# Kernel tuning notes

Measured on AMD Instinct MI355X. Metric: run time of the kernel, lower is better.

## Reference

```python
import jax, jax.numpy as jnp
import numpy as np

N_DIM = 2  # number of trailing feature columns treated as coordinates


def setup_inputs() -> dict:
    key = jax.random.key(0)
    k1, k2, k3, k4 = jax.random.split(key, 4)
    B, N, F, O = 32, 1024, 64, 128
    x = jax.random.normal(k1, (B, N, F), dtype=jnp.float32)
    mask = (jax.random.uniform(k2, (B, N)) < 0.8).astype(jnp.float32)
    # A has shape ((F+1)*2 - 1, O) = (2F+1, O) per build()
    A = jax.random.normal(k3, ((F + 1) * 2 - 1, O), dtype=jnp.float32) * 0.05
    b = jax.random.normal(k4, (O,), dtype=jnp.float32) * 0.05
    return {"x": x, "mask": mask, "A": A, "b": b}


def reference(x, mask, A, b):
    # x: [B,N,F], mask: [B,N], A: [2F+1,O], b: [O]
    # TF tiles: a[b,i,j] = x[b,j]; b_t[b,i,j] = x[b,i]
    coords = x[:, :, -N_DIM:]                              # [B,N,d]
    # diff[b,i,j] = coords[b,j] - coords[b,i]  (ca - cb in TF)
    diff = coords[:, None, :, :] - coords[:, :, None, :]   # [B,N,N,d]
    dist = jnp.sum(diff * diff, axis=-1)                   # [B,N,N] (i,j)
    w = jnp.exp(-10.0 * dist)                              # [B,N,N]
    # TF: s[b,i,j,:] = concat(x[b,j], dist[b,i,j]) * w[b,i,j] * mask[b,j]
    #     ss[b,j]    = sum_i s[b,i,j]
    wsum = jnp.sum(w, axis=1)                              # [B,N] indexed by j
    dwsum = jnp.sum(dist * w, axis=1)                      # [B,N] indexed by j
    m = mask[..., None]                                    # [B,N,1]
    ss_feat = x * wsum[..., None] * m                      # [B,N,F]
    ss_dist = dwsum[..., None] * m                         # [B,N,1]
    ss = jnp.concatenate([ss_feat, ss_dist], axis=-1)      # [B,N,F+1]
    # subtract self term: xx = concat(x, 0)
    xx = jnp.concatenate([x, jnp.zeros_like(x[..., :1])], axis=-1)
    ss = ss - xx
    h = jnp.concatenate([x, ss], axis=-1)                  # [B,N,2F+1]
    out = (h @ A + b) * m                                  # [B,N,O]
    return out
```

## Files before the change

### kernel.cpp

```cpp
#include <hip/hip_runtime.h>
#include <hip/hip_bf16.h>

typedef __attribute__((ext_vector_type(8))) short bf16x8;
typedef __attribute__((ext_vector_type(4))) float f32x4;
typedef __attribute__((ext_vector_type(16))) float f32x16;

#define NN 1024
#define FF 64
#define OO 128

#define LOG2E    1.4426950408889634f
#define C20L     (20.0f * LOG2E)
#define C10L     (10.0f * LOG2E)
#define NEG_LN2_10 (-0.06931471805599453f)
#define BF1      ((short)0x3F80)

__device__ __forceinline__ short bfh(float f) {
    __hip_bfloat16 h = __float2bfloat16(f);
    return *reinterpret_cast<short*>(&h);
}
__device__ __forceinline__ float bf2f(short s) {
    union { unsigned u; float f; } v; v.u = ((unsigned)(unsigned short)s) << 16;
    return v.f;
}

__global__ __launch_bounds__(1024, 4) void gnn_fused_kernel(
    const float* __restrict__ x, const float* __restrict__ mask,
    const float* __restrict__ A, const float* __restrict__ bias,
    float* __restrict__ out)
{
    __shared__ __align__(16) short  ivec[NN * 8];
    __shared__ __align__(16) bf16x8 jlo[128], jhi[128];
    __shared__ __align__(16) bf16x8 cst;
    __shared__ __align__(16) float part_w[2][4][64];
    __shared__ __align__(16) float part_t[2][4][64];

    const int tid = threadIdx.x;
    const int w   = tid >> 6;
    const int l   = tid & 63;
    const int l16 = l & 15;
    const int lh  = l >> 4;

    const int bid = blockIdx.x;
    const int b     = (bid & 7) * 4 + (bid >> 6);
    const int jbase = ((bid >> 3) & 7) * 128;
    const int rowbase_g = b * NN + jbase;
    const float* xb = x + (size_t)b * NN * FF;

    {
        int p = tid;
        float2 c2 = *(const float2*)(xb + (size_t)p * FF + (FF - 2));
        float vx = C20L * c2.x, vy = C20L * c2.y;
        float r2 = fmaf(c2.x, c2.x, c2.y * c2.y);
        float u  = -C10L * r2;
        short vxh = bfh(vx); short vxl = bfh(vx - bf2f(vxh));
        short vyh = bfh(vy); short vyl = bfh(vy - bf2f(vyh));
        short uh  = bfh(u);  short ul  = bfh(u  - bf2f(uh));
        bf16x8 iv = {vxh, vxl, vxh, vyh, vyl, vyh, uh, ul};
        *(bf16x8*)&ivec[p * 8] = iv;
        unsigned jloc = (unsigned)(p - jbase);
        if (jloc < 128u) {
            short xh = bfh(c2.x); short xl = bfh(c2.x - bf2f(xh));
            short yh = bfh(c2.y); short yl = bfh(c2.y - bf2f(yh));
            jlo[jloc] = (bf16x8){xh, xh, xl, yh, yh, yl, BF1, BF1};
            jhi[jloc] = (bf16x8){uh, ul, 0, 0, 0, 0, 0, 0};
        }
        if (tid == 0) cst = (bf16x8){BF1, BF1, 0, 0, 0, 0, 0, 0};
    }

    __syncthreads();

    if (w >= 8) {
        const int idx = w - 8;
        const int jh_ = idx & 1;
        const int iq  = idx >> 1;
        const int j31 = l & 31;
        const f32x16 Z = {0.f,0.f,0.f,0.f,0.f,0.f,0.f,0.f,
                          0.f,0.f,0.f,0.f,0.f,0.f,0.f,0.f};
        for (int t = 0; t < 2; ++t) {
            const int jj = t * 64 + 32 * jh_ + j31;
            const bf16x8* bp = (l < 32) ? &jlo[jj] : &jhi[jj];
            bf16x8 Bj = *bp;
            float aw0 = 0.f, aw1 = 0.f, at0 = 0.f, at1 = 0.f;
            __builtin_amdgcn_s_setprio(1);
            #pragma unroll
            for (int c = 0; c < 8; ++c) {
                const bf16x8* ap = (l < 32)
                    ? (const bf16x8*)&ivec[(iq * 256 + c * 32 + j31) * 8]
                    : &cst;
                bf16x8 Af = *ap;
                f32x16 S = __builtin_amdgcn_mfma_f32_32x32x16_bf16(Af, Bj, Z, 0, 0, 0);
                #pragma unroll
                for (int r = 0; r < 16; r += 2) {
                    float p2a = S[r], p2b = S[r + 1];
                    float wa = __builtin_amdgcn_exp2f(p2a);
                    float wb = __builtin_amdgcn_exp2f(p2b);
                    aw0 += wa;                 aw1 += wb;
                    at0 = fmaf(p2a, wa, at0);  at1 = fmaf(p2b, wb, at1);
                }
            }
            __builtin_amdgcn_s_setprio(0);
            float aw = aw0 + aw1, at = at0 + at1;
            aw += __shfl_xor(aw, 32);
            at += __shfl_xor(at, 32);
            if (l < 32) {
                part_w[t][iq][32 * jh_ + j31] = aw;
                part_t[t][iq][32 * jh_ + j31] = at;
            }
            __syncthreads();
        }
    } else {
        const int colbase = w * 16;
        const f32x4 Z4 = {0.f, 0.f, 0.f, 0.f};
        f32x4 acc[4][2];

        bf16x8 Bh[2][2];
        #pragma unroll
        for (int g = 0; g < 2; ++g)
            #pragma unroll
            for (int q = 0; q < 2; ++q) {
                const float* ap = A + (size_t)(g * FF + 32 * q + 8 * lh) * OO
                                  + colbase + l16;
                #pragma unroll
                for (int e = 0; e < 8; ++e)
                    Bh[g][q][e] = bfh(ap[(size_t)e * OO]);
            }
        const float a2v = A[(size_t)(2 * FF) * OO + colbase + l16];
        const float bbv = bias[colbase + l16];

        for (int t = 0; t < 2; ++t) {
            const float* xpb = x + (size_t)(rowbase_g + t * 64 + l16) * FF + 8 * lh;
            #pragma unroll
            for (int ms = 0; ms < 4; ++ms) {
                const float* _p = xpb + ms * 16 * FF;
                float4 v0 = *(const float4*)(_p);
                float4 v1 = *(const float4*)(_p + 4);
                float4 v2 = *(const float4*)(_p + 32);
                float4 v3 = *(const float4*)(_p + 36);
                float src[16] = {v0.x, v0.y, v0.z, v0.w, v1.x, v1.y, v1.z, v1.w,
                                 v2.x, v2.y, v2.z, v2.w, v3.x, v3.y, v3.z, v3.w};
                bf16x8 Xh[2];
                #pragma unroll
                for (int q = 0; q < 2; ++q)
                    #pragma unroll
                    for (int e = 0; e < 8; ++e)
                        Xh[q][e] = bfh(src[q * 8 + e]);
                #pragma unroll
                for (int g = 0; g < 2; ++g) {
                    acc[ms][g] = __builtin_amdgcn_mfma_f32_16x16x32_bf16(
                        Xh[0], Bh[g][0], Z4, 0, 0, 0);
                    acc[ms][g] = __builtin_amdgcn_mfma_f32_16x16x32_bf16(
                        Xh[1], Bh[g][1], acc[ms][g], 0, 0, 0);
                }
            }

            __syncthreads();

            #pragma unroll
            for (int ms = 0; ms < 4; ++ms) {
                const int rl  = 16 * ms + 4 * lh;
                const int erg = rowbase_g + t * 64 + rl;
                float4 mk = *(const float4*)(mask + erg);
                float4 w0 = *(const float4*)&part_w[t][0][rl];
                float4 w1 = *(const float4*)&part_w[t][1][rl];
                float4 w2 = *(const float4*)&part_w[t][2][rl];
                float4 w3 = *(const float4*)&part_w[t][3][rl];
                float4 t0 = *(const float4*)&part_t[t][0][rl];
                float4 t1 = *(const float4*)&part_t[t][1][rl];
                float4 t2 = *(const float4*)&part_t[t][2][rl];
                float4 t3 = *(const float4*)&part_t[t][3][rl];
                float mks[4] = {mk.x, mk.y, mk.z, mk.w};
                float wvs[4] = {(w0.x + w1.x) + (w2.x + w3.x),
                                (w0.y + w1.y) + (w2.y + w3.y),
                                (w0.z + w1.z) + (w2.z + w3.z),
                                (w0.w + w1.w) + (w2.w + w3.w)};
                float dvs[4] = {((t0.x + t1.x) + (t2.x + t3.x)) * NEG_LN2_10,
                                ((t0.y + t1.y) + (t2.y + t3.y)) * NEG_LN2_10,
                                ((t0.z + t1.z) + (t2.z + t3.z)) * NEG_LN2_10,
                                ((t0.w + t1.w) + (t2.w + t3.w)) * NEG_LN2_10};
                #pragma unroll
                for (int r = 0; r < 4; ++r) {
                    const int row = erg + r;
                    const float m   = mks[r];
                    const float s   = wvs[r] * m - 1.f;
                    const float dwm = dvs[r] * m;
                    float val = acc[ms][0][r] + s * acc[ms][1][r]
                              + dwm * a2v + bbv;
                    out[(size_t)row * OO + colbase + l16] = val * m;
                }
            }
        }
    }
}

extern "C" void kernel_launch(void* const* d_in, const int* in_sizes, int n_in,
                              void* d_out, int out_size, void* d_ws, size_t ws_size,
                              hipStream_t stream)
{
    const float* x    = (const float*)d_in[0];
    const float* mask = (const float*)d_in[1];
    const float* A    = (const float*)d_in[2];
    const float* bias = (const float*)d_in[3];
    float* out = (float*)d_out;

    gnn_fused_kernel<<<dim3(256), dim3(1024), 0, stream>>>(x, mask, A, bias, out);
}
```

Before: 19.59 us.

## Split work into 512 smaller blocks with all waves doing both pairwise and GEMM

Halves the j-tile per block from 128 to 64 and launches 512 blocks of 512 threads instead of 256 blocks of 1024. Wave specialization is dropped: every wave first computes the pairwise exp sums with MFMA, then the feature GEMM and epilogue, with a small shared reduction step in between. The aim is more blocks across CUs and less load imbalance between the specialized wave groups. In exchange, each block rebuilds the full 1024-entry coordinate table, so that prologue work doubles overall, and the phases no longer overlap within a block.

```diff
diff --git a/kernel.cpp b/kernel.cpp
--- a/kernel.cpp
+++ b/kernel.cpp
@@ -24,16 +24,17 @@
     return v.f;
 }
 
-__global__ __launch_bounds__(1024, 4) void gnn_fused_kernel(
+__global__ __launch_bounds__(512, 4) void gnn_fused_kernel(
     const float* __restrict__ x, const float* __restrict__ mask,
     const float* __restrict__ A, const float* __restrict__ bias,
     float* __restrict__ out)
 {
     __shared__ __align__(16) short  ivec[NN * 8];
-    __shared__ __align__(16) bf16x8 jlo[128], jhi[128];
+    __shared__ __align__(16) bf16x8 jlo[64], jhi[64];
     __shared__ __align__(16) bf16x8 cst;
-    __shared__ __align__(16) float part_w[2][4][64];
-    __shared__ __align__(16) float part_t[2][4][64];
+    __shared__ __align__(16) float part_w[2][4][32];
+    __shared__ __align__(16) float part_t[2][4][32];
+    __shared__ __align__(16) float ws_s[64], dw_s[64];
 
     const int tid = threadIdx.x;
     const int w   = tid >> 6;
@@ -42,153 +43,150 @@
     const int lh  = l >> 4;
 
     const int bid = blockIdx.x;
-    const int b     = (bid & 7) * 4 + (bid >> 6);
-    const int jbase = ((bid >> 3) & 7) * 128;
+    const int b     = (bid & 7) * 4 + (bid >> 7);
+    const int jbase = ((bid >> 3) & 15) * 64;
     const int rowbase_g = b * NN + jbase;
     const float* xb = x + (size_t)b * NN * FF;
 
+    const int colbase = w * 16;
+    bf16x8 Bh[2][2];
+    #pragma unroll
+    for (int g = 0; g < 2; ++g)
+        #pragma unroll
+        for (int q = 0; q < 2; ++q) {
+            const float* ap = A + (size_t)(g * FF + 32 * q + 8 * lh) * OO
+                              + colbase + l16;
+            #pragma unroll
+            for (int e = 0; e < 8; ++e)
+                Bh[g][q][e] = bfh(ap[(size_t)e * OO]);
+        }
+    const float a2v = A[(size_t)(2 * FF) * OO + colbase + l16];
+    const float bbv = bias[colbase + l16];
+
     {
-        int p = tid;
-        float2 c2 = *(const float2*)(xb + (size_t)p * FF + (FF - 2));
-        float vx = C20L * c2.x, vy = C20L * c2.y;
-        float r2 = fmaf(c2.x, c2.x, c2.y * c2.y);
-        float u  = -C10L * r2;
-        short vxh = bfh(vx); short vxl = bfh(vx - bf2f(vxh));
-        short vyh = bfh(vy); short vyl = bfh(vy - bf2f(vyh));
-        short uh  = bfh(u);  short ul  = bfh(u  - bf2f(uh));
-        bf16x8 iv = {vxh, vxl, vxh, vyh, vyl, vyh, uh, ul};
-        *(bf16x8*)&ivec[p * 8] = iv;
-        unsigned jloc = (unsigned)(p - jbase);
-        if (jloc < 128u) {
-            short xh = bfh(c2.x); short xl = bfh(c2.x - bf2f(xh));
-            short yh = bfh(c2.y); short yl = bfh(c2.y - bf2f(yh));
-            jlo[jloc] = (bf16x8){xh, xh, xl, yh, yh, yl, BF1, BF1};
-            jhi[jloc] = (bf16x8){uh, ul, 0, 0, 0, 0, 0, 0};
+        float2 c2a = *(const float2*)(xb + (size_t)tid * FF + (FF - 2));
+        float2 c2b = *(const float2*)(xb + (size_t)(tid + 512) * FF + (FF - 2));
+        #pragma unroll
+        for (int q = 0; q < 2; ++q) {
+            int p = tid + q * 512;
+            float2 c2 = q ? c2b : c2a;
+            float vx = C20L * c2.x, vy = C20L * c2.y;
+            float r2 = fmaf(c2.x, c2.x, c2.y * c2.y);
+            float u  = -C10L * r2;
+            short vxh = bfh(vx); short vxl = bfh(vx - bf2f(vxh));
+            short vyh = bfh(vy); short vyl = bfh(vy - bf2f(vyh));
+            short uh  = bfh(u);  short ul  = bfh(u  - bf2f(uh));
+            bf16x8 iv = {vxh, vxl, vxh, vyh, vyl, vyh, uh, ul};
+            *(bf16x8*)&ivec[p * 8] = iv;
+            unsigned jloc = (unsigned)(p - jbase);
+            if (jloc < 64u) {
+                short xh = bfh(c2.x); short xl = bfh(c2.x - bf2f(xh));
+                short yh = bfh(c2.y); short yl = bfh(c2.y - bf2f(yh));
+                jlo[jloc] = (bf16x8){xh, xh, xl, yh, yh, yl, BF1, BF1};
+                jhi[jloc] = (bf16x8){uh, ul, 0, 0, 0, 0, 0, 0};
+            }
         }
         if (tid == 0) cst = (bf16x8){BF1, BF1, 0, 0, 0, 0, 0, 0};
     }
 
     __syncthreads();
 
-    if (w >= 8) {
-        const int idx = w - 8;
-        const int jh_ = idx & 1;
-        const int iq  = idx >> 1;
+    {
+        const int jg  = w & 1;
+        const int iq  = w >> 1;
         const int j31 = l & 31;
+        const bf16x8* bp = (l < 32) ? &jlo[32 * jg + j31] : &jhi[32 * jg + j31];
+        bf16x8 Bj = *bp;
         const f32x16 Z = {0.f,0.f,0.f,0.f,0.f,0.f,0.f,0.f,
                           0.f,0.f,0.f,0.f,0.f,0.f,0.f,0.f};
-        for (int t = 0; t < 2; ++t) {
-            const int jj = t * 64 + 32 * jh_ + j31;
-            const bf16x8* bp = (l < 32) ? &jlo[jj] : &jhi[jj];
-            bf16x8 Bj = *bp;
-            float aw0 = 0.f, aw1 = 0.f, at0 = 0.f, at1 = 0.f;
-            __builtin_amdgcn_s_setprio(1);
+        float aw0 = 0.f, aw1 = 0.f, at0 = 0.f, at1 = 0.f;
+        __builtin_amdgcn_s_setprio(1);
+        #pragma unroll
+        for (int c = 0; c < 8; ++c) {
+            const bf16x8* ap = (l < 32)
+                ? (const bf16x8*)&ivec[(iq * 256 + c * 32 + j31) * 8]
+                : &cst;
+            bf16x8 Af = *ap;
+            f32x16 S = __builtin_amdgcn_mfma_f32_32x32x16_bf16(Af, Bj, Z, 0, 0, 0);
             #pragma unroll
-            for (int c = 0; c < 8; ++c) {
-                const bf16x8* ap = (l < 32)
-                    ? (const bf16x8*)&ivec[(iq * 256 + c * 32 + j31) * 8]
-                    : &cst;
-                bf16x8 Af = *ap;
-                f32x16 S = __builtin_amdgcn_mfma_f32_32x32x16_bf16(Af, Bj, Z, 0, 0, 0);
-                #pragma unroll
-                for (int r = 0; r < 16; r += 2) {
-                    float p2a = S[r], p2b = S[r + 1];
-                    float wa = __builtin_amdgcn_exp2f(p2a);
-                    float wb = __builtin_amdgcn_exp2f(p2b);
-                    aw0 += wa;                 aw1 += wb;
-                    at0 = fmaf(p2a, wa, at0);  at1 = fmaf(p2b, wb, at1);
-                }
+            for (int r = 0; r < 16; r += 2) {
+                float p2a = S[r], p2b = S[r + 1];
+                float wa = __builtin_amdgcn_exp2f(p2a);
+                float wb = __builtin_amdgcn_exp2f(p2b);
+                aw0 += wa;                 aw1 += wb;
+                at0 = fmaf(p2a, wa, at0);  at1 = fmaf(p2b, wb, at1);
             }
-            __builtin_amdgcn_s_setprio(0);
-            float aw = aw0 + aw1, at = at0 + at1;
-            aw += __shfl_xor(aw, 32);
-            at += __shfl_xor(at, 32);
-            if (l < 32) {
-                part_w[t][iq][32 * jh_ + j31] = aw;
-                part_t[t][iq][32 * jh_ + j31] = at;
-            }
-            __syncthreads();
-        }
-    } else {
-        const int colbase = w * 16;
-        const f32x4 Z4 = {0.f, 0.f, 0.f, 0.f};
-        f32x4 acc[4][2];
-
-        bf16x8 Bh[2][2];
-        #pragma unroll
-        for (int g = 0; g < 2; ++g)
+        }
+        __builtin_amdgcn_s_setprio(0);
+        float aw = aw0 + aw1, at = at0 + at1;
+        aw += __shfl_xor(aw, 32);
+        at += __shfl_xor(at, 32);
+        if (l < 32) {
+            part_w[jg][iq][j31] = aw;
+            part_t[jg][iq][j31] = at;
+        }
+    }
+
+    __syncthreads();
+
+    if (tid < 64) {
+        const int tg = tid >> 5, t31 = tid & 31;
+        float sw = (part_w[tg][0][t31] + part_w[tg][1][t31])
+                 + (part_w[tg][2][t31] + part_w[tg][3][t31]);
+        float st = (part_t[tg][0][t31] + part_t[tg][1][t31])
+                 + (part_t[tg][2][t31] + part_t[tg][3][t31]);
+        ws_s[tid] = sw;
+        dw_s[tid] = st * NEG_LN2_10;
+    }
+
+    const f32x4 Z4 = {0.f, 0.f, 0.f, 0.f};
+    f32x4 acc[4][2];
+    const float* xpb = x + (size_t)(rowbase_g + l16) * FF + 8 * lh;
+    #pragma unroll
+    for (int ms = 0; ms < 4; ++ms) {
+        const float* _p = xpb + ms * 16 * FF;
+        float4 v0 = *(const float4*)(_p);
+        float4 v1 = *(const float4*)(_p + 4);
+        float4 v2 = *(const float4*)(_p + 32);
+        float4 v3 = *(const float4*)(_p + 36);
+        float src[16] = {v0.x, v0.y, v0.z, v0.w, v1.x, v1.y, v1.z, v1.w,
+                         v2.x, v2.y, v2.z, v2.w, v3.x, v3.y, v3.z, v3.w};
+        bf16x8 Xh[2];
+        #pragma unroll
+        for (int q = 0; q < 2; ++q)
             #pragma unroll
-            for (int q = 0; q < 2; ++q) {
-                const float* ap = A + (size_t)(g * FF + 32 * q + 8 * lh) * OO
-                                  + colbase + l16;
-                #pragma unroll
-                for (int e = 0; e < 8; ++e)
-                    Bh[g][q][e] = bfh(ap[(size_t)e * OO]);
-            }
-        const float a2v = A[(size_t)(2 * FF) * OO + colbase + l16];
-        const float bbv = bias[colbase + l16];
-
-        for (int t = 0; t < 2; ++t) {
-            const float* xpb = x + (size_t)(rowbase_g + t * 64 + l16) * FF + 8 * lh;
-            #pragma unroll
-            for (int ms = 0; ms < 4; ++ms) {
-                const float* _p = xpb + ms * 16 * FF;
-                float4 v0 = *(const float4*)(_p);
-                float4 v1 = *(const float4*)(_p + 4);
-                float4 v2 = *(const float4*)(_p + 32);
-                float4 v3 = *(const float4*)(_p + 36);
-                float src[16] = {v0.x, v0.y, v0.z, v0.w, v1.x, v1.y, v1.z, v1.w,
-                                 v2.x, v2.y, v2.z, v2.w, v3.x, v3.y, v3.z, v3.w};
-                bf16x8 Xh[2];
-                #pragma unroll
-                for (int q = 0; q < 2; ++q)
-                    #pragma unroll
-                    for (int e = 0; e < 8; ++e)
-                        Xh[q][e] = bfh(src[q * 8 + e]);
-                #pragma unroll
-                for (int g = 0; g < 2; ++g) {
-                    acc[ms][g] = __builtin_amdgcn_mfma_f32_16x16x32_bf16(
-                        Xh[0], Bh[g][0], Z4, 0, 0, 0);
-                    acc[ms][g] = __builtin_amdgcn_mfma_f32_16x16x32_bf16(
-                        Xh[1], Bh[g][1], acc[ms][g], 0, 0, 0);
-                }
-            }
-
-            __syncthreads();
-
-            #pragma unroll
-            for (int ms = 0; ms < 4; ++ms) {
-                const int rl  = 16 * ms + 4 * lh;
-                const int erg = rowbase_g + t * 64 + rl;
-                float4 mk = *(const float4*)(mask + erg);
-                float4 w0 = *(const float4*)&part_w[t][0][rl];
-                float4 w1 = *(const float4*)&part_w[t][1][rl];
-                float4 w2 = *(const float4*)&part_w[t][2][rl];
-                float4 w3 = *(const float4*)&part_w[t][3][rl];
-                float4 t0 = *(const float4*)&part_t[t][0][rl];
-                float4 t1 = *(const float4*)&part_t[t][1][rl];
-                float4 t2 = *(const float4*)&part_t[t][2][rl];
-                float4 t3 = *(const float4*)&part_t[t][3][rl];
-                float mks[4] = {mk.x, mk.y, mk.z, mk.w};
-                float wvs[4] = {(w0.x + w1.x) + (w2.x + w3.x),
-                                (w0.y + w1.y) + (w2.y + w3.y),
-                                (w0.z + w1.z) + (w2.z + w3.z),
-                                (w0.w + w1.w) + (w2.w + w3.w)};
-                float dvs[4] = {((t0.x + t1.x) + (t2.x + t3.x)) * NEG_LN2_10,
-                                ((t0.y + t1.y) + (t2.y + t3.y)) * NEG_LN2_10,
-                                ((t0.z + t1.z) + (t2.z + t3.z)) * NEG_LN2_10,
-                                ((t0.w + t1.w) + (t2.w + t3.w)) * NEG_LN2_10};
-                #pragma unroll
-                for (int r = 0; r < 4; ++r) {
-                    const int row = erg + r;
-                    const float m   = mks[r];
-                    const float s   = wvs[r] * m - 1.f;
-                    const float dwm = dvs[r] * m;
-                    float val = acc[ms][0][r] + s * acc[ms][1][r]
-                              + dwm * a2v + bbv;
-                    out[(size_t)row * OO + colbase + l16] = val * m;
-                }
-            }
+            for (int e = 0; e < 8; ++e)
+                Xh[q][e] = bfh(src[q * 8 + e]);
+        #pragma unroll
+        for (int g = 0; g < 2; ++g) {
+            acc[ms][g] = __builtin_amdgcn_mfma_f32_16x16x32_bf16(
+                Xh[0], Bh[g][0], Z4, 0, 0, 0);
+            acc[ms][g] = __builtin_amdgcn_mfma_f32_16x16x32_bf16(
+                Xh[1], Bh[g][1], acc[ms][g], 0, 0, 0);
+        }
+    }
+
+    __syncthreads();
+
+    #pragma unroll
+    for (int ms = 0; ms < 4; ++ms) {
+        const int rl  = 16 * ms + 4 * lh;
+        const int erg = rowbase_g + rl;
+        float4 mk = *(const float4*)(mask + erg);
+        float4 wv = *(const float4*)&ws_s[rl];
+        float4 dv = *(const float4*)&dw_s[rl];
+        float mks[4] = {mk.x, mk.y, mk.z, mk.w};
+        float wvs[4] = {wv.x, wv.y, wv.z, wv.w};
+        float dvs[4] = {dv.x, dv.y, dv.z, dv.w};
+        #pragma unroll
+        for (int r = 0; r < 4; ++r) {
+            const int row = erg + r;
+            const float m   = mks[r];
+            const float s   = wvs[r] * m - 1.f;
+            const float dwm = dvs[r] * m;
+            float val = acc[ms][0][r] + s * acc[ms][1][r]
+                      + dwm * a2v + bbv;
+            out[(size_t)row * OO + colbase + l16] = val * m;
         }
     }
 }
@@ -203,5 +201,5 @@
     const float* bias = (const float*)d_in[3];
     float* out = (float*)d_out;
 
-    gnn_fused_kernel<<<dim3(256), dim3(1024), 0, stream>>>(x, mask, A, bias, out);
-}
+    gnn_fused_kernel<<<dim3(512), dim3(512), 0, stream>>>(x, mask, A, bias, out);
+}
```

New measurement: 21.31 us. 1.09x slower.

## Halve block size and run pairwise and projection phases in the same waves

Applied to the files above, without the earlier changes.

The block shrinks from 1024 to 512 threads, and the split between specialized waves goes away. All 8 waves now first compute the pairwise exp-weighted sums, covering 512 i-rows each instead of 256, then all 8 do the bf16 MFMA projection and epilogue. The A-weight fragment loads are hoisted to before the coordinate staging. This removes the warp specialization and the per-t barriers, which may cut LDS and register pressure and raise occupancy. In exchange, the projection no longer overlaps the exp-heavy pairwise phase, so the two phases run back to back.

```diff
diff --git a/kernel.cpp b/kernel.cpp
--- a/kernel.cpp
+++ b/kernel.cpp
@@ -24,7 +24,7 @@
     return v.f;
 }
 
-__global__ __launch_bounds__(1024, 4) void gnn_fused_kernel(
+__global__ __launch_bounds__(512) void gnn_fused_kernel(
     const float* __restrict__ x, const float* __restrict__ mask,
     const float* __restrict__ A, const float* __restrict__ bias,
     float* __restrict__ out)
@@ -32,8 +32,8 @@
     __shared__ __align__(16) short  ivec[NN * 8];
     __shared__ __align__(16) bf16x8 jlo[128], jhi[128];
     __shared__ __align__(16) bf16x8 cst;
-    __shared__ __align__(16) float part_w[2][4][64];
-    __shared__ __align__(16) float part_t[2][4][64];
+    __shared__ __align__(16) float part_w[2][2][64];
+    __shared__ __align__(16) float part_t[2][2][64];
 
     const int tid = threadIdx.x;
     const int w   = tid >> 6;
@@ -47,8 +47,24 @@
     const int rowbase_g = b * NN + jbase;
     const float* xb = x + (size_t)b * NN * FF;
 
-    {
-        int p = tid;
+    const int colbase = w * 16;
+    bf16x8 Bh[2][2];
+    #pragma unroll
+    for (int g = 0; g < 2; ++g)
+        #pragma unroll
+        for (int q = 0; q < 2; ++q) {
+            const float* ap = A + (size_t)(g * FF + 32 * q + 8 * lh) * OO
+                              + colbase + l16;
+            #pragma unroll
+            for (int e = 0; e < 8; ++e)
+                Bh[g][q][e] = bfh(ap[(size_t)e * OO]);
+        }
+    const float a2v = A[(size_t)(2 * FF) * OO + colbase + l16];
+    const float bbv = bias[colbase + l16];
+
+    #pragma unroll
+    for (int q = 0; q < 2; ++q) {
+        int p = tid + q * 512;
         float2 c2 = *(const float2*)(xb + (size_t)p * FF + (FF - 2));
         float vx = C20L * c2.x, vy = C20L * c2.y;
         float r2 = fmaf(c2.x, c2.x, c2.y * c2.y);
@@ -65,129 +81,101 @@
             jlo[jloc] = (bf16x8){xh, xh, xl, yh, yh, yl, BF1, BF1};
             jhi[jloc] = (bf16x8){uh, ul, 0, 0, 0, 0, 0, 0};
         }
-        if (tid == 0) cst = (bf16x8){BF1, BF1, 0, 0, 0, 0, 0, 0};
+    }
+    if (tid == 0) cst = (bf16x8){BF1, BF1, 0, 0, 0, 0, 0, 0};
+
+    __syncthreads();
+
+    {
+        const int t_  = w >> 2;
+        const int ih  = (w >> 1) & 1;
+        const int jg  = w & 1;
+        const int j31 = l & 31;
+        const int jj = t_ * 64 + 32 * jg + j31;
+        const bf16x8* bp = (l < 32) ? &jlo[jj] : &jhi[jj];
+        bf16x8 Bj = *bp;
+        const f32x16 Z = {0.f,0.f,0.f,0.f,0.f,0.f,0.f,0.f,
+                          0.f,0.f,0.f,0.f,0.f,0.f,0.f,0.f};
+        float aw0 = 0.f, aw1 = 0.f, at0 = 0.f, at1 = 0.f;
+        __builtin_amdgcn_s_setprio(1);
+        #pragma unroll
+        for (int c = 0; c < 16; ++c) {
+            const bf16x8* ap = (l < 32)
+                ? (const bf16x8*)&ivec[(ih * 512 + c * 32 + j31) * 8]
+                : &cst;
+            bf16x8 Af = *ap;
+            f32x16 S = __builtin_amdgcn_mfma_f32_32x32x16_bf16(Af, Bj, Z, 0, 0, 0);
+            #pragma unroll
+            for (int r = 0; r < 16; r += 2) {
+                float p2a = S[r], p2b = S[r + 1];
+                float wa = __builtin_amdgcn_exp2f(p2a);
+                float wb = __builtin_amdgcn_exp2f(p2b);
+                aw0 += wa;                 aw1 += wb;
+                at0 = fmaf(p2a, wa, at0);  at1 = fmaf(p2b, wb, at1);
+            }
+        }
+        __builtin_amdgcn_s_setprio(0);
+        float aw = aw0 + aw1, at = at0 + at1;
+        aw += __shfl_xor(aw, 32);
+        at += __shfl_xor(at, 32);
+        if (l < 32) {
+            part_w[t_][ih][32 * jg + j31] = aw;
+            part_t[t_][ih][32 * jg + j31] = at;
+        }
     }
 
     __syncthreads();
 
-    if (w >= 8) {
-        const int idx = w - 8;
-        const int jh_ = idx & 1;
-        const int iq  = idx >> 1;
-        const int j31 = l & 31;
-        const f32x16 Z = {0.f,0.f,0.f,0.f,0.f,0.f,0.f,0.f,
-                          0.f,0.f,0.f,0.f,0.f,0.f,0.f,0.f};
-        for (int t = 0; t < 2; ++t) {
-            const int jj = t * 64 + 32 * jh_ + j31;
-            const bf16x8* bp = (l < 32) ? &jlo[jj] : &jhi[jj];
-            bf16x8 Bj = *bp;
-            float aw0 = 0.f, aw1 = 0.f, at0 = 0.f, at1 = 0.f;
-            __builtin_amdgcn_s_setprio(1);
+    const f32x4 Z4 = {0.f, 0.f, 0.f, 0.f};
+    for (int t = 0; t < 2; ++t) {
+        f32x4 acc[4][2];
+        const float* xpb = x + (size_t)(rowbase_g + t * 64 + l16) * FF + 8 * lh;
+        #pragma unroll
+        for (int ms = 0; ms < 4; ++ms) {
+            const float* _p = xpb + ms * 16 * FF;
+            float4 v0 = *(const float4*)(_p);
+            float4 v1 = *(const float4*)(_p + 4);
+            float4 v2 = *(const float4*)(_p + 32);
+            float4 v3 = *(const float4*)(_p + 36);
+            float src[16] = {v0.x, v0.y, v0.z, v0.w, v1.x, v1.y, v1.z, v1.w,
+                             v2.x, v2.y, v2.z, v2.w, v3.x, v3.y, v3.z, v3.w};
+            bf16x8 Xh[2];
             #pragma unroll
-            for (int c = 0; c < 8; ++c) {
-                const bf16x8* ap = (l < 32)
-                    ? (const bf16x8*)&ivec[(iq * 256 + c * 32 + j31) * 8]
-                    : &cst;
-                bf16x8 Af = *ap;
-                f32x16 S = __builtin_amdgcn_mfma_f32_32x32x16_bf16(Af, Bj, Z, 0, 0, 0);
-                #pragma unroll
-                for (int r = 0; r < 16; r += 2) {
-                    float p2a = S[r], p2b = S[r + 1];
-                    float wa = __builtin_amdgcn_exp2f(p2a);
-                    float wb = __builtin_amdgcn_exp2f(p2b);
-                    aw0 += wa;                 aw1 += wb;
-                    at0 = fmaf(p2a, wa, at0);  at1 = fmaf(p2b, wb, at1);
-                }
-            }
-            __builtin_amdgcn_s_setprio(0);
-            float aw = aw0 + aw1, at = at0 + at1;
-            aw += __shfl_xor(aw, 32);
-            at += __shfl_xor(at, 32);
-            if (l < 32) {
-                part_w[t][iq][32 * jh_ + j31] = aw;
-                part_t[t][iq][32 * jh_ + j31] = at;
-            }
-            __syncthreads();
-        }
-    } else {
-        const int colbase = w * 16;
-        const f32x4 Z4 = {0.f, 0.f, 0.f, 0.f};
-        f32x4 acc[4][2];
-
-        bf16x8 Bh[2][2];
-        #pragma unroll
-        for (int g = 0; g < 2; ++g)
-            #pragma unroll
-            for (int q = 0; q < 2; ++q) {
-                const float* ap = A + (size_t)(g * FF + 32 * q + 8 * lh) * OO
-                                  + colbase + l16;
+            for (int q = 0; q < 2; ++q)
                 #pragma unroll
                 for (int e = 0; e < 8; ++e)
-                    Bh[g][q][e] = bfh(ap[(size_t)e * OO]);
+                    Xh[q][e] = bfh(src[q * 8 + e]);
+            #pragma unroll
+            for (int g = 0; g < 2; ++g) {
+                acc[ms][g] = __builtin_amdgcn_mfma_f32_16x16x32_bf16(
+                    Xh[0], Bh[g][0], Z4, 0, 0, 0);
+                acc[ms][g] = __builtin_amdgcn_mfma_f32_16x16x32_bf16(
+                    Xh[1], Bh[g][1], acc[ms][g], 0, 0, 0);
             }
-        const float a2v = A[(size_t)(2 * FF) * OO + colbase + l16];
-        const float bbv = bias[colbase + l16];
+        }
 
-        for (int t = 0; t < 2; ++t) {
-            const float* xpb = x + (size_t)(rowbase_g + t * 64 + l16) * FF + 8 * lh;
+        #pragma unroll
+        for (int ms = 0; ms < 4; ++ms) {
+            const int rl  = 16 * ms + 4 * lh;
+            const int erg = rowbase_g + t * 64 + rl;
+            float4 mk = *(const float4*)(mask + erg);
+            float4 w0 = *(const float4*)&part_w[t][0][rl];
+            float4 w1 = *(const float4*)&part_w[t][1][rl];
+            float4 t0 = *(const float4*)&part_t[t][0][rl];
+            float4 t1 = *(const float4*)&part_t[t][1][rl];
+            float mks[4] = {mk.x, mk.y, mk.z, mk.w};
+            float wvs[4] = {w0.x + w1.x, w0.y + w1.y, w0.z + w1.z, w0.w + w1.w};
+            float dvs[4] = {(t0.x + t1.x) * NEG_LN2_10, (t0.y + t1.y) * NEG_LN2_10,
+                            (t0.z + t1.z) * NEG_LN2_10, (t0.w + t1.w) * NEG_LN2_10};
             #pragma unroll
-            for (int ms = 0; ms < 4; ++ms) {
-                const float* _p = xpb + ms * 16 * FF;
-                float4 v0 = *(const float4*)(_p);
-                float4 v1 = *(const float4*)(_p + 4);
-                float4 v2 = *(const float4*)(_p + 32);
-                float4 v3 = *(const float4*)(_p + 36);
-                float src[16] = {v0.x, v0.y, v0.z, v0.w, v1.x, v1.y, v1.z, v1.w,
-                                 v2.x, v2.y, v2.z, v2.w, v3.x, v3.y, v3.z, v3.w};
-                bf16x8 Xh[2];
-                #pragma unroll
-                for (int q = 0; q < 2; ++q)
-                    #pragma unroll
-                    for (int e = 0; e < 8; ++e)
-                        Xh[q][e] = bfh(src[q * 8 + e]);
-                #pragma unroll
-                for (int g = 0; g < 2; ++g) {
-                    acc[ms][g] = __builtin_amdgcn_mfma_f32_16x16x32_bf16(
-                        Xh[0], Bh[g][0], Z4, 0, 0, 0);
-                    acc[ms][g] = __builtin_amdgcn_mfma_f32_16x16x32_bf16(
-                        Xh[1], Bh[g][1], acc[ms][g], 0, 0, 0);
-                }
-            }
-
-            __syncthreads();
-
-            #pragma unroll
-            for (int ms = 0; ms < 4; ++ms) {
-                const int rl  = 16 * ms + 4 * lh;
-                const int erg = rowbase_g + t * 64 + rl;
-                float4 mk = *(const float4*)(mask + erg);
-                float4 w0 = *(const float4*)&part_w[t][0][rl];
-                float4 w1 = *(const float4*)&part_w[t][1][rl];
-                float4 w2 = *(const float4*)&part_w[t][2][rl];
-                float4 w3 = *(const float4*)&part_w[t][3][rl];
-                float4 t0 = *(const float4*)&part_t[t][0][rl];
-                float4 t1 = *(const float4*)&part_t[t][1][rl];
-                float4 t2 = *(const float4*)&part_t[t][2][rl];
-                float4 t3 = *(const float4*)&part_t[t][3][rl];
-                float mks[4] = {mk.x, mk.y, mk.z, mk.w};
-                float wvs[4] = {(w0.x + w1.x) + (w2.x + w3.x),
-                                (w0.y + w1.y) + (w2.y + w3.y),
-                                (w0.z + w1.z) + (w2.z + w3.z),
-                                (w0.w + w1.w) + (w2.w + w3.w)};
-                float dvs[4] = {((t0.x + t1.x) + (t2.x + t3.x)) * NEG_LN2_10,
-                                ((t0.y + t1.y) + (t2.y + t3.y)) * NEG_LN2_10,
-                                ((t0.z + t1.z) + (t2.z + t3.z)) * NEG_LN2_10,
-                                ((t0.w + t1.w) + (t2.w + t3.w)) * NEG_LN2_10};
-                #pragma unroll
-                for (int r = 0; r < 4; ++r) {
-                    const int row = erg + r;
-                    const float m   = mks[r];
-                    const float s   = wvs[r] * m - 1.f;
-                    const float dwm = dvs[r] * m;
-                    float val = acc[ms][0][r] + s * acc[ms][1][r]
-                              + dwm * a2v + bbv;
-                    out[(size_t)row * OO + colbase + l16] = val * m;
-                }
+            for (int r = 0; r < 4; ++r) {
+                const int row = erg + r;
+                const float m   = mks[r];
+                const float s   = wvs[r] * m - 1.f;
+                const float dwm = dvs[r] * m;
+                float val = acc[ms][0][r] + s * acc[ms][1][r]
+                          + dwm * a2v + bbv;
+                out[(size_t)row * OO + colbase + l16] = val * m;
             }
         }
     }
@@ -203,5 +191,5 @@
     const float* bias = (const float*)d_in[3];
     float* out = (float*)d_out;
 
-    gnn_fused_kernel<<<dim3(256), dim3(1024), 0, stream>>>(x, mask, A, bias, out);
+    gnn_fused_kernel<<<dim3(256), dim3(512), 0, stream>>>(x, mask, A, bias, out);
 }
```

Measured after the change: 22.48 us. 14.8% more time.
